# Performance work log

Measured on AMD Instinct MI355X. Metric: run time of the kernel, lower is better.

Reference implementation:

```python
import jax, jax.numpy as jnp
import numpy as np

B_, L_, H_ = 2, 2048, 2048          # batch, seq_len, hidden_size
I_, N_, NH, P_ = 4096, 128, 64, 64   # intermediate, ssm_state, num_heads, head_dim
K_, CH = 4, 256                      # conv kernel, chunk size
DT_MIN, DT_MAX = 0.0, 1e10


def setup_inputs() -> dict:
    key = jax.random.key(0)
    ks = jax.random.split(key, 8)
    conv_dim = I_ + 2 * N_
    proj_out = 2 * (I_ + N_) + NH
    return {
        "hidden_states": jax.random.normal(ks[0], (B_, L_, H_), jnp.float32),
        "W_in": jax.random.normal(ks[1], (proj_out, H_), jnp.float32) * 0.02,
        "conv_w": jax.random.normal(ks[2], (conv_dim, 1, K_), jnp.float32) * 0.2,
        "conv_b": jnp.zeros((conv_dim,), jnp.float32),
        "dt_bias": jax.random.uniform(ks[3], (NH,), jnp.float32),
        "A_log": jnp.log(jax.random.uniform(ks[4], (NH,), jnp.float32, 1.0, 16.0)),
        "D": jnp.ones((NH,), jnp.float32),
        "norm_w": jnp.ones((I_,), jnp.float32),
        "W_out": jax.random.normal(ks[5], (H_, I_), jnp.float32) * 0.02,
    }


def _segsum(x):
    # stable segment-sum: out[..., i, j] = sum_{k=j+1..i} x[..., k] for i>=j, else -inf
    T = x.shape[-1]
    xr = jnp.broadcast_to(x[..., None], x.shape + (T,))
    lower = jnp.tril(jnp.ones((T, T), bool), -1)
    s = jnp.cumsum(jnp.where(lower, xr, 0.0), axis=-2)
    return jnp.where(jnp.tril(jnp.ones((T, T), bool)), s, -jnp.inf)


def reference(hidden_states, W_in, conv_w, conv_b, dt_bias, A_log, D, norm_w, W_out):
    b, L, _ = hidden_states.shape
    proj = hidden_states @ W_in.T                       # (b, L, 2*(I+N)+H)
    z, xBC, dt = jnp.split(proj, [I_, 2 * I_ + 2 * N_], axis=-1)

    # depthwise causal conv1d + silu
    x_t = xBC.transpose(0, 2, 1)                        # (b, conv_dim, L)
    conv = jax.lax.conv_general_dilated(
        x_t, conv_w, (1,), [(K_ - 1, 0)],
        dimension_numbers=("NCH", "OIH", "NCH"), feature_group_count=I_ + 2 * N_)
    xBC = jax.nn.silu((conv + conv_b[None, :, None]).transpose(0, 2, 1))
    x, Bm, Cm = jnp.split(xBC, [I_, I_ + N_], axis=-1)  # (b,L,I) (b,L,N) (b,L,N)

    # ---- SSD naive (chunked state-space-duality scan) ----
    A = -jnp.exp(A_log.astype(jnp.float32))             # (h,)
    dt = jnp.clip(jax.nn.softplus(dt + dt_bias), DT_MIN, DT_MAX)  # (b,L,h)
    x4 = x.reshape(b, L, NH, P_)
    pad = (-L) % CH
    padf = lambda t: jnp.pad(t, [(0, 0), (0, pad)] + [(0, 0)] * (t.ndim - 2))
    D_res = D[None, None, :, None] * padf(x4)           # (b, Lp, h, p)
    xs = padf(x4 * dt[..., None])
    Ah = padf(A[None, None, :] * dt)                    # (b, Lp, h)
    Bc, Cc = padf(Bm), padf(Cm)
    c = (L + pad) // CH
    xs = xs.reshape(b, c, CH, NH, P_)                   # (b,c,l,h,p)
    Ah = Ah.reshape(b, c, CH, NH).transpose(0, 3, 1, 2) # (b,h,c,l)
    Bc = Bc.reshape(b, c, CH, N_)
    Cc = Cc.reshape(b, c, CH, N_)

    A_cs = jnp.cumsum(Ah, axis=-1)                      # (b,h,c,l)
    Lm = jnp.exp(_segsum(Ah))                           # (b,h,c,l,l)
    # intra-chunk (diagonal block) output; B/C shared across heads (n_groups=1)
    Y_diag = jnp.einsum("bcln,bcsn,bhcls,bcshp->bclhp", Cc, Bc, Lm, xs)

    decay_states = jnp.exp(A_cs[..., -1:] - A_cs)       # (b,h,c,l)
    states = jnp.einsum("bcln,bhcl,bclhp->bchpn", Bc, decay_states, xs)
    states = jnp.concatenate([jnp.zeros_like(states[:, :1]), states], axis=1)
    decay_chunk = jnp.exp(_segsum(jnp.pad(A_cs[..., -1], [(0, 0), (0, 0), (1, 0)])))
    new_states = jnp.einsum("bhzc,bchpn->bzhpn", decay_chunk, states)
    states = new_states[:, :-1]                         # (b,c,h,p,n)
    Y_off = jnp.einsum("bcln,bchpn,bhcl->bclhp", Cc, states, jnp.exp(A_cs))

    y = (Y_diag + Y_off).reshape(b, c * CH, NH, P_) + D_res
    y = y[:, :L].reshape(b, L, I_)

    # gated RMSNorm (normalize=True: multiply by silu(residual) before norm)
    yf = y.astype(jnp.float32) * jax.nn.silu(z.astype(jnp.float32))
    yf = yf * jax.lax.rsqrt(jnp.mean(yf * yf, -1, keepdims=True) + 1e-5) * norm_w
    return yf.astype(hidden_states.dtype) @ W_out.T
```

## Files before the change

kernel.cpp:

```cpp
#include <hip/hip_runtime.h>
#include <hip/hip_bf16.h>
#include <math.h>


#define B_SZ 2
#define L_SZ 2048
#define H_SZ 2048
#define I_SZ 4096
#define N_SZ 128
#define NH_SZ 64
#define P_SZ 64
#define CH_SZ 256
#define NC_SZ 8
#define PROJ_SZ 8512
#define CONV_SZ 4352
#define XOFF 4096
#define DTOFF 8448
#define BOFF 4096
#define COFF 4224

typedef __attribute__((ext_vector_type(8))) short short8_t;
typedef __attribute__((ext_vector_type(4))) float float4_t;

#define GLDS(gp, lp)                                                   \
  __builtin_amdgcn_global_load_lds(                                    \
      (const __attribute__((address_space(1))) void*)(gp),             \
      (__attribute__((address_space(3))) void*)(lp), 16, 0, 0)

__device__ __forceinline__ float bf2f(unsigned short u) {
  union { unsigned int i; float f; } v; v.i = ((unsigned int)u) << 16; return v.f;
}
__device__ __forceinline__ unsigned short f2bf(float f) {
  union { float f; unsigned int i; } v; v.f = f;
  unsigned int b = v.i + 0x7fffu + ((v.i >> 16) & 1u);
  return (unsigned short)(b >> 16);
}
__device__ __forceinline__ void unpack8(uint4 v, float* f) {
  f[0] = bf2f((unsigned short)(v.x & 0xffffu)); f[1] = bf2f((unsigned short)(v.x >> 16));
  f[2] = bf2f((unsigned short)(v.y & 0xffffu)); f[3] = bf2f((unsigned short)(v.y >> 16));
  f[4] = bf2f((unsigned short)(v.z & 0xffffu)); f[5] = bf2f((unsigned short)(v.z >> 16));
  f[6] = bf2f((unsigned short)(v.w & 0xffffu)); f[7] = bf2f((unsigned short)(v.w >> 16));
}
__device__ __forceinline__ float silu_f(float x) { return x / (1.f + expf(-x)); }

__device__ __forceinline__ float load1(const void* p, long long e, int fp32) {
  return fp32 ? ((const float*)p)[e] : bf2f(((const unsigned short*)p)[e]);
}
__device__ __forceinline__ void load4(const void* p, long long e, int fp32, float* f) {
  if (fp32) {
    float4 a = *(const float4*)((const float*)p + e);
    f[0] = a.x; f[1] = a.y; f[2] = a.z; f[3] = a.w;
  } else {
    uint2 v = *(const uint2*)((const unsigned short*)p + e);
    f[0] = bf2f((unsigned short)(v.x & 0xffffu)); f[1] = bf2f((unsigned short)(v.x >> 16));
    f[2] = bf2f((unsigned short)(v.y & 0xffffu)); f[3] = bf2f((unsigned short)(v.y >> 16));
  }
}
__device__ __forceinline__ void load8(const void* p, long long e, int fp32, float* f) {
  if (fp32) {
    float4 a = *(const float4*)((const float*)p + e);
    float4 b = *(const float4*)((const float*)p + e + 4);
    f[0] = a.x; f[1] = a.y; f[2] = a.z; f[3] = a.w;
    f[4] = b.x; f[5] = b.y; f[6] = b.z; f[7] = b.w;
  } else {
    uint4 v = *(const uint4*)((const unsigned short*)p + e);
    unpack8(v, f);
  }
}

__global__ void detect_k(const void* p0, const void* p1, const void* p2,
                         const void* p3, const void* p4, const void* p5,
                         const void* p6, const void* p7, const void* p8,
                         int n0, int n1, int n2, int n3, int n4, int n5,
                         int n6, int n7, int n8, int* flags) {
  __shared__ int pe, po;
  const void* ps[9] = {p0, p1, p2, p3, p4, p5, p6, p7, p8};
  int ns[9] = {n0, n1, n2, n3, n4, n5, n6, n7, n8};
  int t = threadIdx.x;
  for (int i = 0; i < 9; i++) {
    if (t == 0) { pe = 0; po = 0; }
    __syncthreads();
    int S = ns[i] < 256 ? ns[i] : 256;
    if (t < S) {
      unsigned short u = ((const unsigned short*)ps[i])[t];
      int ex = (u >> 7) & 0xFF;
      int plaus = ((u & 0x7FFFu) != 0) && (ex >= 0x70) && (ex <= 0x8F);
      if (plaus) { if (t & 1) atomicAdd(&po, 1); else atomicAdd(&pe, 1); }
    }
    __syncthreads();
    if (t == 0) flags[i] = (2 * pe < po) ? 1 : 0;
    __syncthreads();
  }
  if (t == 0) { flags[14] = 0; flags[15] = 0; }
}

__global__ __launch_bounds__(256)
void cvt_bf16_k(const void* __restrict__ src, unsigned short* __restrict__ dst,
                long long n8, const int* __restrict__ flags, int fi) {
  long long g = (long long)blockIdx.x * 256 + threadIdx.x;
  if (g >= n8) return;
  long long e = g * 8;
  if (flags[fi]) {
    const float* s = (const float*)src + e;
    float4 a = *(const float4*)s;
    float4 b = *(const float4*)(s + 4);
    unsigned short o[8] = {f2bf(a.x), f2bf(a.y), f2bf(a.z), f2bf(a.w),
                           f2bf(b.x), f2bf(b.y), f2bf(b.z), f2bf(b.w)};
    *(uint4*)(dst + e) = *(const uint4*)o;
  } else {
    *(uint4*)(dst + e) = *(const uint4*)((const unsigned short*)src + e);
  }
}

#define MFMA_ACC(d, a, b) \
  d = __builtin_amdgcn_mfma_f32_16x16x32_bf16(a, b, d, 0, 0, 0)
#define LDA_FR(buf, i, kk) \
  (*(const short8_t*)&As[(buf)*16384 + (wm*128 + (i)*16 + l16)*64 + \
                         (((((kk)<<2) + quad) ^ l7) << 3)])
#define LDB_FR(buf, j, kk) \
  (*(const short8_t*)&Bs[(buf)*16384 + (wn*64 + (j)*16 + l16)*64 + \
                         (((((kk)<<2) + quad) ^ l7) << 3)])
#define STAGE_A(h, tile, buf) do {                                          \
    GLDS(aSrc[h][0] + ((long long)(tile) << 6),                             \
         &As[(buf)*16384 + (h)*8192 + (wave*16)*64]);                       \
    GLDS(aSrc[h][1] + ((long long)(tile) << 6),                             \
         &As[(buf)*16384 + (h)*8192 + (wave*16 + 8)*64]);                   \
  } while (0)
#define STAGE_B(h, tile, buf) do {                                          \
    GLDS(bSrc[h][0] + ((long long)(tile) << 6),                             \
         &Bs[(buf)*16384 + (h)*8192 + (wave*16)*64]);                       \
    GLDS(bSrc[h][1] + ((long long)(tile) << 6),                             \
         &Bs[(buf)*16384 + (h)*8192 + (wave*16 + 8)*64]);                   \
  } while (0)

__global__ __launch_bounds__(512, 2)
void gemm_8ph_k(const unsigned short* __restrict__ A,
                const unsigned short* __restrict__ B,
                unsigned short* __restrict__ C,
                int N, int K, int lda, int ldb, int ldc, int gxTiles) {
  __shared__ alignas(16) unsigned short As[2 * 256 * 64];
  __shared__ alignas(16) unsigned short Bs[2 * 256 * 64];
  const int t = threadIdx.x;
  const int lane = t & 63;
  const int wave = t >> 6;
  const int quad = lane >> 4;
  const int l16 = lane & 15;
  const int l7 = lane & 7;
  const int l3 = lane >> 3;
  const int wm = wave >> 2;
  const int wn = wave & 3;

  int id = blockIdx.x;
  const int nwg = gridDim.x;
  int swz = id;
  if ((nwg & 7) == 0) swz = (id & 7) * (nwg >> 3) + (id >> 3);
  const int band = gxTiles << 2;
  const int by = (swz & 3) + ((swz / band) << 2);
  const int bx = (swz >> 2) % gxTiles;
  const int m0 = by << 8;
  const int n0 = bx << 8;
  const int NT = K >> 6;

  const int kperm = ((l7 ^ l3) << 3);
  const unsigned short* aSrc[2][2];
  const unsigned short* bSrc[2][2];
#pragma unroll
  for (int h = 0; h < 2; ++h)
#pragma unroll
    for (int c = 0; c < 2; ++c) {
      const int rloc = h * 128 + wave * 16 + c * 8 + l3;
      aSrc[h][c] = A + (long long)(m0 + rloc) * lda + kperm;
      int bn = n0 + rloc;
      if (bn > N - 1) bn = N - 1;
      bSrc[h][c] = B + (long long)bn * ldb + kperm;
    }

  float4_t acc[8][4];
#pragma unroll
  for (int i = 0; i < 8; ++i)
#pragma unroll
    for (int j = 0; j < 4; ++j) acc[i][j] = (float4_t){0.f, 0.f, 0.f, 0.f};

  STAGE_A(0, 0, 0); STAGE_A(1, 0, 0);
  STAGE_B(0, 0, 0); STAGE_B(1, 0, 0);
  STAGE_B(0, 1, 1); STAGE_B(1, 1, 1);
  asm volatile("s_waitcnt vmcnt(4)" ::: "memory");
  __builtin_amdgcn_s_barrier();

  short8_t af[4][2], bf[4][2];
  for (int tt = 0; tt < NT; ++tt) {
    const int rb = tt & 1, nb = rb ^ 1;
#pragma unroll
    for (int i = 0; i < 4; ++i) af[i][0] = LDA_FR(rb, i, 0);
#pragma unroll
    for (int j = 0; j < 4; ++j) bf[j][0] = LDB_FR(rb, j, 0);
    if (tt + 1 < NT) STAGE_A(0, tt + 1, nb);
    asm volatile("s_waitcnt lgkmcnt(4)" ::: "memory");
    __builtin_amdgcn_s_barrier();
    asm volatile("s_waitcnt lgkmcnt(0)" ::: "memory");
    __builtin_amdgcn_s_setprio(1);
#pragma unroll
    for (int i = 0; i < 4; ++i)
#pragma unroll
      for (int j = 0; j < 4; ++j) MFMA_ACC(acc[i][j], af[i][0], bf[j][0]);
    __builtin_amdgcn_s_setprio(0);
    __builtin_amdgcn_s_barrier();
#pragma unroll
    for (int i = 0; i < 4; ++i) af[i][1] = LDA_FR(rb, i, 1);
#pragma unroll
    for (int j = 0; j < 4; ++j) bf[j][1] = LDB_FR(rb, j, 1);
    if (tt + 1 < NT) STAGE_A(1, tt + 1, nb);
    asm volatile("s_waitcnt lgkmcnt(4)" ::: "memory");
    __builtin_amdgcn_s_barrier();
    asm volatile("s_waitcnt lgkmcnt(0)" ::: "memory");
    __builtin_amdgcn_s_setprio(1);
#pragma unroll
    for (int i = 0; i < 4; ++i)
#pragma unroll
      for (int j = 0; j < 4; ++j) MFMA_ACC(acc[i][j], af[i][1], bf[j][1]);
    __builtin_amdgcn_s_setprio(0);
    __builtin_amdgcn_s_barrier();
#pragma unroll
    for (int i = 0; i < 4; ++i) af[i][0] = LDA_FR(rb, 4 + i, 0);
    if (tt + 2 < NT) STAGE_B(0, tt + 2, rb);
    __builtin_amdgcn_s_barrier();
    asm volatile("s_waitcnt lgkmcnt(0)" ::: "memory");
    __builtin_amdgcn_s_setprio(1);
#pragma unroll
    for (int i = 0; i < 4; ++i)
#pragma unroll
      for (int j = 0; j < 4; ++j) MFMA_ACC(acc[4 + i][j], af[i][0], bf[j][0]);
    __builtin_amdgcn_s_setprio(0);
    __builtin_amdgcn_s_barrier();
#pragma unroll
    for (int i = 0; i < 4; ++i) af[i][1] = LDA_FR(rb, 4 + i, 1);
    if (tt + 2 < NT) STAGE_B(1, tt + 2, rb);
    __builtin_amdgcn_s_barrier();
    asm volatile("s_waitcnt lgkmcnt(0)" ::: "memory");
    __builtin_amdgcn_s_setprio(1);
#pragma unroll
    for (int i = 0; i < 4; ++i)
#pragma unroll
      for (int j = 0; j < 4; ++j) MFMA_ACC(acc[4 + i][j], af[i][1], bf[j][1]);
    __builtin_amdgcn_s_setprio(0);
    if (tt < NT - 2) asm volatile("s_waitcnt vmcnt(4)" ::: "memory");
    else             asm volatile("s_waitcnt vmcnt(0)" ::: "memory");
    __builtin_amdgcn_s_barrier();
  }

#pragma unroll
  for (int i = 0; i < 8; ++i) {
#pragma unroll
    for (int r = 0; r < 4; ++r) {
      const int m = m0 + wm * 128 + i * 16 + quad * 4 + r;
      const long long cb = (long long)m * ldc;
#pragma unroll
      for (int j = 0; j < 4; ++j) {
        const int n = n0 + wn * 64 + j * 16 + l16;
        if (n < N) C[cb + n] = f2bf(acc[i][j][r]);
      }
    }
  }
}

#define LDA2(buf, i, kk) \
  (*(const short8_t*)&As2[(buf)*8192 + (wm*64 + (i)*16 + l16)*64 + \
                          (((((kk)<<2) + quad) ^ l7) << 3)])
#define LDB2(buf, j, kk) \
  (*(const short8_t*)&Bs2[(buf)*8192 + (wn*64 + (j)*16 + l16)*64 + \
                          (((((kk)<<2) + quad) ^ l7) << 3)])

template <int OUT_MODE>
__global__ __launch_bounds__(256, 2)
void gemm_2ph_k(const unsigned short* __restrict__ A,
                const unsigned short* __restrict__ B,
                void* __restrict__ Cptr,
                int N, int K, int lda, int ldb, int ldc, int gxTiles,
                const int* __restrict__ flags, int fo) {
  __shared__ alignas(16) unsigned short As2[2 * 128 * 64];
  __shared__ alignas(16) unsigned short Bs2[2 * 128 * 64];
  const int t = threadIdx.x;
  const int lane = t & 63;
  const int wave = t >> 6;
  const int quad = lane >> 4;
  const int l16 = lane & 15;
  const int l7 = lane & 7;
  const int l3 = lane >> 3;
  const int wm = wave >> 1;
  const int wn = wave & 1;
  const int ofp = (OUT_MODE == 2) ? flags[fo] : 0;

  int id = blockIdx.x;
  const int nwg = gridDim.x;
  int swz = id;
  if ((nwg & 7) == 0) swz = (id & 7) * (nwg >> 3) + (id >> 3);
  const int band = gxTiles << 2;
  const int by = (swz & 3) + ((swz / band) << 2);
  const int bx = (swz >> 2) % gxTiles;
  const int m0 = by << 7;
  const int n0 = bx << 7;
  const int NT = K >> 6;

  const int kperm = ((l7 ^ l3) << 3);
  const unsigned short* aSrc[4];
  const unsigned short* bSrc[4];
#pragma unroll
  for (int c = 0; c < 4; ++c) {
    aSrc[c] = A + (long long)(m0 + wave * 32 + c * 8 + l3) * lda + kperm;
    int bn = n0 + wave * 32 + c * 8 + l3;
    if (bn > N - 1) bn = N - 1;
    bSrc[c] = B + (long long)bn * ldb + kperm;
  }

  float4_t acc[4][4];
#pragma unroll
  for (int i = 0; i < 4; ++i)
#pragma unroll
    for (int j = 0; j < 4; ++j) acc[i][j] = (float4_t){0.f, 0.f, 0.f, 0.f};

#pragma unroll
  for (int c = 0; c < 4; ++c) {
    GLDS(aSrc[c], &As2[(wave * 32 + c * 8) * 64]);
    GLDS(bSrc[c], &Bs2[(wave * 32 + c * 8) * 64]);
  }
  asm volatile("s_waitcnt vmcnt(0)" ::: "memory");
  __builtin_amdgcn_s_barrier();

  short8_t af[4], bfr[4];
  for (int tt = 0; tt < NT; ++tt) {
    const int rb = tt & 1, nb = rb ^ 1;
#pragma unroll
    for (int i = 0; i < 4; ++i) af[i] = LDA2(rb, i, 0);
#pragma unroll
    for (int j = 0; j < 4; ++j) bfr[j] = LDB2(rb, j, 0);
    if (tt + 1 < NT) {
      const long long ko = (long long)(tt + 1) << 6;
#pragma unroll
      for (int c = 0; c < 4; ++c) {
        GLDS(aSrc[c] + ko, &As2[nb * 8192 + (wave * 32 + c * 8) * 64]);
        GLDS(bSrc[c] + ko, &Bs2[nb * 8192 + (wave * 32 + c * 8) * 64]);
      }
    }
    __builtin_amdgcn_s_setprio(1);
#pragma unroll
    for (int i = 0; i < 4; ++i)
#pragma unroll
      for (int j = 0; j < 4; ++j) MFMA_ACC(acc[i][j], af[i], bfr[j]);
    __builtin_amdgcn_s_setprio(0);
#pragma unroll
    for (int i = 0; i < 4; ++i) af[i] = LDA2(rb, i, 1);
#pragma unroll
    for (int j = 0; j < 4; ++j) bfr[j] = LDB2(rb, j, 1);
    __builtin_amdgcn_s_setprio(1);
#pragma unroll
    for (int i = 0; i < 4; ++i)
#pragma unroll
      for (int j = 0; j < 4; ++j) MFMA_ACC(acc[i][j], af[i], bfr[j]);
    __builtin_amdgcn_s_setprio(0);
    asm volatile("s_waitcnt vmcnt(0)" ::: "memory");
    __builtin_amdgcn_s_barrier();
  }

#pragma unroll
  for (int i = 0; i < 4; ++i) {
#pragma unroll
    for (int r = 0; r < 4; ++r) {
      const int m = m0 + wm * 64 + i * 16 + quad * 4 + r;
      const long long cb = (long long)m * ldc;
#pragma unroll
      for (int j = 0; j < 4; ++j) {
        const int n = n0 + wn * 64 + j * 16 + l16;
        if (n < N) {
          float v = acc[i][j][r];
          if (ofp) ((float*)Cptr)[cb + n] = v;
          else     ((unsigned short*)Cptr)[cb + n] = f2bf(v);
        }
      }
    }
  }
}

template <int OUT_MODE>
__global__ __launch_bounds__(256)
void gemm_bt_k(const void* __restrict__ A, const void* __restrict__ B,
               void* __restrict__ Cptr, int M, int N, int K,
               int lda, int ldb, int ldc,
               long long sA, long long sB, long long sC,
               const int* __restrict__ flags, int fa, int fb, int fo) {
  __shared__ float As[128][20];
  __shared__ float Bs[128][20];
  const int t = threadIdx.x;
  const int tx = t & 15, ty = t >> 4;
  const int m0 = blockIdx.y * 128, n0 = blockIdx.x * 128;
  const int afp = flags[fa], bfp = flags[fb];
  const int ofp = (OUT_MODE == 2) ? flags[fo] : (OUT_MODE == 1);
  const long long zoff = (long long)blockIdx.z;
  float* Cf = (float*)Cptr + zoff * sC;
  unsigned short* Cb = (unsigned short*)Cptr + zoff * sC;

  float acc[8][8];
#pragma unroll
  for (int i = 0; i < 8; i++)
#pragma unroll
    for (int j = 0; j < 8; j++) acc[i][j] = 0.f;

  const int rowS = t >> 1;
  const int kof  = (t & 1) * 8;
  const long long aRow = zoff * sA + (long long)(m0 + rowS) * lda + kof;
  const long long bRow = zoff * sB + (long long)(n0 + rowS) * ldb + kof;
  const bool bOK = (n0 + rowS) < N;

  for (int k0 = 0; k0 < K; k0 += 16) {
    float af[8], bf[8];
    load8(A, aRow + k0, afp, af);
    if (bOK) load8(B, bRow + k0, bfp, bf);
    else { bf[0]=bf[1]=bf[2]=bf[3]=bf[4]=bf[5]=bf[6]=bf[7]=0.f; }
    __syncthreads();
    *(float4*)&As[rowS][kof]     = make_float4(af[0], af[1], af[2], af[3]);
    *(float4*)&As[rowS][kof + 4] = make_float4(af[4], af[5], af[6], af[7]);
    *(float4*)&Bs[rowS][kof]     = make_float4(bf[0], bf[1], bf[2], bf[3]);
    *(float4*)&Bs[rowS][kof + 4] = make_float4(bf[4], bf[5], bf[6], bf[7]);
    __syncthreads();
#pragma unroll
    for (int kk = 0; kk < 16; kk += 2) {
      float2 a2[8], b2[8];
#pragma unroll
      for (int i = 0; i < 8; i++) a2[i] = *(const float2*)&As[ty + 16 * i][kk];
#pragma unroll
      for (int j = 0; j < 8; j++) b2[j] = *(const float2*)&Bs[tx + 16 * j][kk];
#pragma unroll
      for (int i = 0; i < 8; i++)
#pragma unroll
        for (int j = 0; j < 8; j++) {
          acc[i][j] = fmaf(a2[i].x, b2[j].x, acc[i][j]);
          acc[i][j] = fmaf(a2[i].y, b2[j].y, acc[i][j]);
        }
    }
  }
#pragma unroll
  for (int i = 0; i < 8; i++) {
    const int m = m0 + ty + 16 * i;
    const long long base = (long long)m * ldc;
#pragma unroll
    for (int j = 0; j < 8; j++) {
      const int n = n0 + tx + 16 * j;
      if (n < N) {
        if (ofp) Cf[base + n] = acc[i][j];
        else     Cb[base + n] = f2bf(acc[i][j]);
      }
    }
  }
}

__global__ __launch_bounds__(256)
void conv_silu_k(const unsigned short* __restrict__ proj,
                 const void* __restrict__ cw,
                 const void* __restrict__ cb,
                 unsigned short* __restrict__ convx,
                 const int* __restrict__ flags) {
  const int total = B_SZ * L_SZ * (CONV_SZ / 4);
  int g = blockIdx.x * 256 + threadIdx.x;
  if (g >= total) return;
  const int fw = flags[2], fb = flags[3];
  int c4 = g % (CONV_SZ / 4);
  int bl = g / (CONV_SZ / 4);
  int l = bl & (L_SZ - 1);
  int ch = c4 * 4;
  float w0[8], w1[8];
  load8(cw, (long long)ch * 4, fw, w0);
  load8(cw, (long long)ch * 4 + 8, fw, w1);
  float accv[4];
  load4(cb, ch, fb, accv);
  float acc0 = accv[0], acc1 = accv[1], acc2 = accv[2], acc3 = accv[3];
  const long long rb = (long long)(bl - l);
#pragma unroll
  for (int k = 0; k < 4; k++) {
    int ls = l - 3 + k;
    if (ls < 0) continue;
    uint2 xv = *(const uint2*)(proj + (rb + ls) * PROJ_SZ + XOFF + ch);
    float x0 = bf2f((unsigned short)(xv.x & 0xffffu));
    float x1 = bf2f((unsigned short)(xv.x >> 16));
    float x2 = bf2f((unsigned short)(xv.y & 0xffffu));
    float x3 = bf2f((unsigned short)(xv.y >> 16));
    acc0 = fmaf(x0, w0[k], acc0);
    acc1 = fmaf(x1, w0[4 + k], acc1);
    acc2 = fmaf(x2, w1[k], acc2);
    acc3 = fmaf(x3, w1[4 + k], acc3);
  }
  unsigned short o0 = f2bf(silu_f(acc0));
  unsigned short o1 = f2bf(silu_f(acc1));
  unsigned short o2 = f2bf(silu_f(acc2));
  unsigned short o3 = f2bf(silu_f(acc3));
  *(uint2*)(convx + (long long)bl * CONV_SZ + ch) =
      make_uint2((unsigned int)o0 | ((unsigned int)o1 << 16),
                 (unsigned int)o2 | ((unsigned int)o3 << 16));
}

__global__ __launch_bounds__(256)
void dt_prep_k(const unsigned short* __restrict__ proj,
               const void* __restrict__ dt_bias,
               float* __restrict__ dtv, const int* __restrict__ flags) {
  int g = blockIdx.x * 256 + threadIdx.x;
  int h = g & 63;
  long long bl = g >> 6;
  float v = bf2f(proj[bl * PROJ_SZ + DTOFF + h]) + load1(dt_bias, h, flags[4]);
  float sp = (v > 20.f) ? v : log1pf(expf(v));
  dtv[g] = sp;
}

__global__ __launch_bounds__(256)
void acs_scan_k(const float* __restrict__ dtv,
                const void* __restrict__ A_log,
                float* __restrict__ acs, const int* __restrict__ flags) {
  __shared__ float sd[256];
  int blk = blockIdx.x;
  int h = blk & 63;
  int bc = blk >> 6;
  int l = threadIdx.x;
  float Ah = -expf(load1(A_log, h, flags[5]));
  long long row = (long long)bc * CH_SZ + l;
  sd[l] = Ah * dtv[row * NH_SZ + h];
  for (int off = 1; off < 256; off <<= 1) {
    __syncthreads();
    float tv = (l >= off) ? sd[l - off] : 0.f;
    __syncthreads();
    sd[l] += tv;
  }
  acs[(long long)blk * CH_SZ + l] = sd[l];
}

__global__ __launch_bounds__(256)
void chunk_states_k(const unsigned short* __restrict__ convx,
                    const float* __restrict__ dtv,
                    const float* __restrict__ acs,
                    float* __restrict__ stc) {
  __shared__ float Bw[32][128];
  __shared__ float xw[32][64];
  int blk = blockIdx.x;
  int h = blk & 63;
  int bc = blk >> 6;
  int t = threadIdx.x;
  const int p0 = (t & 15) * 4, n0 = (t >> 4) * 8;
  const float* acsb = acs + (long long)blk * 256;
  const float alast = acsb[255];
  float acc[4][8];
#pragma unroll
  for (int i = 0; i < 4; i++)
#pragma unroll
    for (int j = 0; j < 8; j++) acc[i][j] = 0.f;
  const long long row0 = (long long)bc * 256;

  for (int lt0 = 0; lt0 < 256; lt0 += 32) {
    __syncthreads();
#pragma unroll
    for (int q = 0; q < 4; q++) {
      int idx4 = (t + 256 * q) * 4;
      int r = idx4 >> 7, n = idx4 & 127;
      uint2 v = *(const uint2*)(convx + (row0 + lt0 + r) * CONV_SZ + BOFF + n);
      Bw[r][n]     = bf2f((unsigned short)(v.x & 0xffffu));
      Bw[r][n + 1] = bf2f((unsigned short)(v.x >> 16));
      Bw[r][n + 2] = bf2f((unsigned short)(v.y & 0xffffu));
      Bw[r][n + 3] = bf2f((unsigned short)(v.y >> 16));
    }
#pragma unroll
    for (int q = 0; q < 2; q++) {
      int idx4 = (t + 256 * q) * 4;
      int r = idx4 >> 6, p = idx4 & 63;
      long long lg = row0 + lt0 + r;
      float sc = dtv[lg * NH_SZ + h] * expf(alast - acsb[lt0 + r]);
      uint2 v = *(const uint2*)(convx + lg * CONV_SZ + h * 64 + p);
      xw[r][p]     = bf2f((unsigned short)(v.x & 0xffffu)) * sc;
      xw[r][p + 1] = bf2f((unsigned short)(v.x >> 16)) * sc;
      xw[r][p + 2] = bf2f((unsigned short)(v.y & 0xffffu)) * sc;
      xw[r][p + 3] = bf2f((unsigned short)(v.y >> 16)) * sc;
    }
    __syncthreads();
#pragma unroll 4
    for (int lt = 0; lt < 32; lt++) {
      float4 xv = *(const float4*)&xw[lt][p0];
      float4 b0 = *(const float4*)&Bw[lt][n0];
      float4 b1 = *(const float4*)&Bw[lt][n0 + 4];
      float xa[4] = {xv.x, xv.y, xv.z, xv.w};
      float ba[8] = {b0.x, b0.y, b0.z, b0.w, b1.x, b1.y, b1.z, b1.w};
#pragma unroll
      for (int i = 0; i < 4; i++)
#pragma unroll
        for (int j = 0; j < 8; j++) acc[i][j] = fmaf(xa[i], ba[j], acc[i][j]);
    }
  }
  float* outb = stc + (long long)blk * 8192;
#pragma unroll
  for (int i = 0; i < 4; i++) {
    *(float4*)&outb[(p0 + i) * 128 + n0] =
        make_float4(acc[i][0], acc[i][1], acc[i][2], acc[i][3]);
    *(float4*)&outb[(p0 + i) * 128 + n0 + 4] =
        make_float4(acc[i][4], acc[i][5], acc[i][6], acc[i][7]);
  }
}

__global__ __launch_bounds__(256)
void recur_k(float* __restrict__ stc, const float* __restrict__ acs) {
  int blk = blockIdx.x;
  int b = blk >> 6, h = blk & 63;
  int t = threadIdx.x;
  float S[32];
#pragma unroll
  for (int j = 0; j < 32; j++) S[j] = 0.f;
  for (int z = 0; z < 8; z++) {
    long long bz = ((long long)b * 8 + z) * 64 + h;
    long long base = bz * 8192;
    float e = expf(acs[bz * 256 + 255]);
#pragma unroll
    for (int j = 0; j < 32; j++) {
      int idx = j * 256 + t;
      float cs = stc[base + idx];
      stc[base + idx] = S[j];
      S[j] = fmaf(e, S[j], cs);
    }
  }
}

__global__ __launch_bounds__(256)
void yoff_k(const unsigned short* __restrict__ convx,
            const float* __restrict__ sti,
            const float* __restrict__ acs,
            const void* __restrict__ Dw,
            float* __restrict__ y, const int* __restrict__ flags) {
  __shared__ float SIt[128][68];
  __shared__ unsigned short Ct[64][128];
  int blk = blockIdx.x;
  int h = blk & 63;
  int bc = blk >> 6;
  int t = threadIdx.x;
  const int txp = t & 15, lq = t >> 4;
  const float Dh = load1(Dw, h, flags[6]);
  const float* sib = sti + (long long)blk * 8192;
#pragma unroll 4
  for (int q = 0; q < 32; q++) {
    int idx = t + 256 * q;
    SIt[idx & 127][idx >> 7] = sib[idx];
  }
  const float* acsb = acs + (long long)blk * 256;
  const long long row0 = (long long)bc * 256;
  for (int ltile = 0; ltile < 4; ltile++) {
    __syncthreads();
#pragma unroll 4
    for (int q = 0; q < 32; q++) {
      int idx = t + 256 * q;
      int lr = idx >> 7, n = idx & 127;
      Ct[lr][n] = convx[(row0 + ltile * 64 + lr) * CONV_SZ + COFF + n];
    }
    __syncthreads();
    float acc[4][4] = {};
#pragma unroll 4
    for (int n = 0; n < 128; n++) {
      float4 sv = *(const float4*)&SIt[n][txp * 4];
      float c0 = bf2f(Ct[lq * 4 + 0][n]);
      float c1 = bf2f(Ct[lq * 4 + 1][n]);
      float c2 = bf2f(Ct[lq * 4 + 2][n]);
      float c3 = bf2f(Ct[lq * 4 + 3][n]);
      acc[0][0] = fmaf(c0, sv.x, acc[0][0]); acc[0][1] = fmaf(c0, sv.y, acc[0][1]);
      acc[0][2] = fmaf(c0, sv.z, acc[0][2]); acc[0][3] = fmaf(c0, sv.w, acc[0][3]);
      acc[1][0] = fmaf(c1, sv.x, acc[1][0]); acc[1][1] = fmaf(c1, sv.y, acc[1][1]);
      acc[1][2] = fmaf(c1, sv.z, acc[1][2]); acc[1][3] = fmaf(c1, sv.w, acc[1][3]);
      acc[2][0] = fmaf(c2, sv.x, acc[2][0]); acc[2][1] = fmaf(c2, sv.y, acc[2][1]);
      acc[2][2] = fmaf(c2, sv.z, acc[2][2]); acc[2][3] = fmaf(c2, sv.w, acc[2][3]);
      acc[3][0] = fmaf(c3, sv.x, acc[3][0]); acc[3][1] = fmaf(c3, sv.y, acc[3][1]);
      acc[3][2] = fmaf(c3, sv.z, acc[3][2]); acc[3][3] = fmaf(c3, sv.w, acc[3][3]);
    }
#pragma unroll
    for (int i = 0; i < 4; i++) {
      int lloc = ltile * 64 + lq * 4 + i;
      long long row = row0 + lloc;
      float ex = expf(acsb[lloc]);
      uint2 xv = *(const uint2*)(convx + row * CONV_SZ + h * 64 + txp * 4);
      float4 o;
      o.x = fmaf(ex, acc[i][0], Dh * bf2f((unsigned short)(xv.x & 0xffffu)));
      o.y = fmaf(ex, acc[i][1], Dh * bf2f((unsigned short)(xv.x >> 16)));
      o.z = fmaf(ex, acc[i][2], Dh * bf2f((unsigned short)(xv.y & 0xffffu)));
      o.w = fmaf(ex, acc[i][3], Dh * bf2f((unsigned short)(xv.y >> 16)));
      *(float4*)&y[row * I_SZ + h * 64 + txp * 4] = o;
    }
  }
}

__global__ __launch_bounds__(256)
void ydiag_k(const unsigned short* __restrict__ convx,
             const float* __restrict__ dtv,
             const float* __restrict__ acs,
             const float* __restrict__ Gmat,
             float* __restrict__ y) {
  __shared__ float acs_s[256];
  __shared__ float xsT[64][68];
  __shared__ float Mt[64][66];
  int blk = blockIdx.x;
  int h = blk & 63;
  int bc = blk >> 6;
  int t = threadIdx.x;
  const int txp = t & 15, lq = t >> 4;
  acs_s[t] = acs[(long long)blk * 256 + t];
  const long long row0 = (long long)bc * 256;
  const float* Gb = Gmat + (long long)bc * 65536;
  for (int ltile = 0; ltile < 4; ltile++) {
    float acc[4][4] = {};
    for (int stile = 0; stile <= ltile; stile++) {
      __syncthreads();
#pragma unroll 4
      for (int q = 0; q < 16; q++) {
        int idx = t + 256 * q;
        int ss = idx >> 6, p = idx & 63;
        long long row = row0 + stile * 64 + ss;
        xsT[ss][p] = bf2f(convx[row * CONV_SZ + h * 64 + p]) * dtv[row * NH_SZ + h];
      }
#pragma unroll 4
      for (int q = 0; q < 16; q++) {
        int idx = t + 256 * q;
        int lr = idx >> 6, ss = idx & 63;
        int lg = ltile * 64 + lr, sg = stile * 64 + ss;
        float m = 0.f;
        if (sg <= lg) m = Gb[(long long)lg * 256 + sg] * expf(acs_s[lg] - acs_s[sg]);
        Mt[lr][ss] = m;
      }
      __syncthreads();
#pragma unroll 4
      for (int ss = 0; ss < 64; ss++) {
        float4 xv = *(const float4*)&xsT[ss][txp * 4];
        float m0 = Mt[lq * 4 + 0][ss];
        float m1 = Mt[lq * 4 + 1][ss];
        float m2 = Mt[lq * 4 + 2][ss];
        float m3 = Mt[lq * 4 + 3][ss];
        acc[0][0] = fmaf(m0, xv.x, acc[0][0]); acc[0][1] = fmaf(m0, xv.y, acc[0][1]);
        acc[0][2] = fmaf(m0, xv.z, acc[0][2]); acc[0][3] = fmaf(m0, xv.w, acc[0][3]);
        acc[1][0] = fmaf(m1, xv.x, acc[1][0]); acc[1][1] = fmaf(m1, xv.y, acc[1][1]);
        acc[1][2] = fmaf(m1, xv.z, acc[1][2]); acc[1][3] = fmaf(m1, xv.w, acc[1][3]);
        acc[2][0] = fmaf(m2, xv.x, acc[2][0]); acc[2][1] = fmaf(m2, xv.y, acc[2][1]);
        acc[2][2] = fmaf(m2, xv.z, acc[2][2]); acc[2][3] = fmaf(m2, xv.w, acc[2][3]);
        acc[3][0] = fmaf(m3, xv.x, acc[3][0]); acc[3][1] = fmaf(m3, xv.y, acc[3][1]);
        acc[3][2] = fmaf(m3, xv.z, acc[3][2]); acc[3][3] = fmaf(m3, xv.w, acc[3][3]);
      }
    }
#pragma unroll
    for (int i = 0; i < 4; i++) {
      long long row = row0 + ltile * 64 + lq * 4 + i;
      float* yp = &y[row * I_SZ + h * 64 + txp * 4];
      float4 cur = *(float4*)yp;
      cur.x += acc[i][0]; cur.y += acc[i][1]; cur.z += acc[i][2]; cur.w += acc[i][3];
      *(float4*)yp = cur;
    }
  }
}

__global__ __launch_bounds__(256)
void norm_k(const float* __restrict__ y,
            const unsigned short* __restrict__ proj,
            const void* __restrict__ nw,
            unsigned short* __restrict__ yfb, const int* __restrict__ flags) {
  __shared__ float red[4];
  __shared__ float sc_s;
  int row = blockIdx.x;
  int t = threadIdx.x;
  const int fn = flags[7];
  const float* yr = y + (long long)row * I_SZ;
  const unsigned short* zr = proj + (long long)row * PROJ_SZ;
  float g[16];
  float ss = 0.f;
#pragma unroll
  for (int q = 0; q < 4; q++) {
    int i0 = q * 1024 + t * 4;
    float4 yv = *(const float4*)&yr[i0];
    uint2 zv = *(const uint2*)&zr[i0];
    float z0 = bf2f((unsigned short)(zv.x & 0xffffu));
    float z1 = bf2f((unsigned short)(zv.x >> 16));
    float z2 = bf2f((unsigned short)(zv.y & 0xffffu));
    float z3 = bf2f((unsigned short)(zv.y >> 16));
    float g0 = yv.x * silu_f(z0), g1 = yv.y * silu_f(z1);
    float g2 = yv.z * silu_f(z2), g3 = yv.w * silu_f(z3);
    g[q * 4 + 0] = g0; g[q * 4 + 1] = g1; g[q * 4 + 2] = g2; g[q * 4 + 3] = g3;
    ss += g0 * g0 + g1 * g1 + g2 * g2 + g3 * g3;
  }
#pragma unroll
  for (int off = 32; off > 0; off >>= 1) ss += __shfl_down(ss, off, 64);
  if ((t & 63) == 0) red[t >> 6] = ss;
  __syncthreads();
  if (t == 0) sc_s = rsqrtf((red[0] + red[1] + red[2] + red[3]) * (1.f / 4096.f) + 1e-5f);
  __syncthreads();
  float sc = sc_s;
#pragma unroll
  for (int q = 0; q < 4; q++) {
    int i0 = q * 1024 + t * 4;
    float nv[4];
    load4(nw, i0, fn, nv);
    unsigned short o0 = f2bf(g[q * 4 + 0] * sc * nv[0]);
    unsigned short o1 = f2bf(g[q * 4 + 1] * sc * nv[1]);
    unsigned short o2 = f2bf(g[q * 4 + 2] * sc * nv[2]);
    unsigned short o3 = f2bf(g[q * 4 + 3] * sc * nv[3]);
    *(uint2*)&yfb[(long long)row * I_SZ + i0] =
        make_uint2((unsigned int)o0 | ((unsigned int)o1 << 16),
                   (unsigned int)o2 | ((unsigned int)o3 << 16));
  }
}

extern "C" void kernel_launch(void* const* d_in, const int* in_sizes, int n_in,
                              void* d_out, int out_size, void* d_ws, size_t ws_size,
                              hipStream_t stream) {
  const void* hs     = d_in[0];
  const void* W_in   = d_in[1];
  const void* conv_w = d_in[2];
  const void* conv_b = d_in[3];
  const void* dt_b   = d_in[4];
  const void* A_log  = d_in[5];
  const void* Dw     = d_in[6];
  const void* nw     = d_in[7];
  const void* W_out  = d_in[8];

  char* ws = (char*)d_ws;
  size_t off = 0;
  auto alloc = [&](size_t bytes) -> void* {
    void* p = ws + off;
    off += (bytes + 255) & ~(size_t)255;
    return p;
  };
  const long long ML = (long long)B_SZ * L_SZ;
  int* flags = (int*)alloc(64);
  unsigned short* proj  = (unsigned short*)alloc(ML * PROJ_SZ * 2);
  unsigned short* convx = (unsigned short*)alloc(ML * CONV_SZ * 2);
  float* dtv  = (float*)alloc(ML * NH_SZ * 4);
  float* acsb = (float*)alloc((long long)B_SZ * NC_SZ * NH_SZ * CH_SZ * 4);
  float* Gm   = (float*)alloc((long long)B_SZ * NC_SZ * CH_SZ * CH_SZ * 4);
  float* stc  = (float*)alloc((long long)B_SZ * NC_SZ * NH_SZ * P_SZ * N_SZ * 4);
  float* yb   = (float*)alloc(ML * I_SZ * 4);
  unsigned short* yfb = (unsigned short*)stc;
  unsigned short* hs_bf   = (unsigned short*)yb;
  unsigned short* Win_bf  = (unsigned short*)yb + 8388608;
  unsigned short* Wout_bf = (unsigned short*)yb;
  (void)n_in; (void)out_size;
  if (off > ws_size) return;

  dim3 blk(256);
  detect_k<<<1, blk, 0, stream>>>(hs, W_in, conv_w, conv_b, dt_b, A_log, Dw, nw, W_out,
                                  in_sizes[0], in_sizes[1], in_sizes[2], in_sizes[3],
                                  in_sizes[4], in_sizes[5], in_sizes[6], in_sizes[7],
                                  in_sizes[8], flags);
  cvt_bf16_k<<<dim3(4096), blk, 0, stream>>>(hs, hs_bf, 1048576LL, flags, 0);
  cvt_bf16_k<<<dim3(8512), blk, 0, stream>>>(W_in, Win_bf, 2179072LL, flags, 1);
  gemm_8ph_k<<<dim3(512), dim3(512), 0, stream>>>(
      hs_bf, Win_bf, proj, PROJ_SZ, H_SZ, H_SZ, H_SZ, PROJ_SZ, 32);
  gemm_2ph_k<0><<<dim3(96), blk, 0, stream>>>(
      hs_bf, Win_bf + 8192LL * 2048, proj + 8192, 320, H_SZ,
      H_SZ, H_SZ, PROJ_SZ, 3, flags, 15);
  conv_silu_k<<<dim3((B_SZ * L_SZ * (CONV_SZ / 4) + 255) / 256), blk, 0, stream>>>(
      proj, conv_w, conv_b, convx, flags);
  dt_prep_k<<<dim3((unsigned)(ML * NH_SZ / 256)), blk, 0, stream>>>(proj, dt_b, dtv, flags);
  acs_scan_k<<<dim3(B_SZ * NC_SZ * NH_SZ), blk, 0, stream>>>(dtv, A_log, acsb, flags);
  gemm_bt_k<1><<<dim3(2, 2, 16), blk, 0, stream>>>(
      (const unsigned short*)convx + COFF, (const unsigned short*)convx + BOFF,
      Gm, 256, 256, 128, CONV_SZ, CONV_SZ, 256,
      (long long)256 * CONV_SZ, (long long)256 * CONV_SZ, 65536,
      flags, 15, 15, 15);
  chunk_states_k<<<dim3(1024), blk, 0, stream>>>(convx, dtv, acsb, stc);
  recur_k<<<dim3(B_SZ * NH_SZ), blk, 0, stream>>>(stc, acsb);
  yoff_k<<<dim3(1024), blk, 0, stream>>>(convx, stc, acsb, Dw, yb, flags);
  ydiag_k<<<dim3(1024), blk, 0, stream>>>(convx, dtv, acsb, Gm, yb);
  norm_k<<<dim3((unsigned)ML), blk, 0, stream>>>(yb, proj, nw, yfb, flags);
  cvt_bf16_k<<<dim3(4096), blk, 0, stream>>>(W_out, Wout_bf, 1048576LL, flags, 8);
  gemm_2ph_k<2><<<dim3(512), blk, 0, stream>>>(
      yfb, Wout_bf, d_out, H_SZ, I_SZ, I_SZ, I_SZ, H_SZ, 16,
      flags, 0);
}
```

Before: 726.9 us.

## Use MFMA for C·B Gram matrix and off-diagonal state output kernels

Replaces the FP32 SIMT tiled GEMM that computes the per-chunk C·Bᵀ Gram matrix with an MFMA kernel that loads bf16 fragments straight from global memory. The Y_off kernel is likewise rewritten to use MFMA, converting the fp32 inter-chunk states to bf16 on the fly instead of staging them transposed in shared memory. This is meant to cut FMA-bound time in two medium-sized GEMMs. In exchange it drops shared-memory reuse, uses less coalesced scalar stores, and rounds the states to bf16, which costs some accuracy.

```diff
diff --git a/kernel.cpp b/kernel.cpp
--- a/kernel.cpp
+++ b/kernel.cpp
@@ -66,6 +66,16 @@
     uint4 v = *(const uint4*)((const unsigned short*)p + e);
     unpack8(v, f);
   }
+}
+__device__ __forceinline__ short8_t pack_bf8(const float* p) {
+  float4 a = *(const float4*)p;
+  float4 b = *(const float4*)(p + 4);
+  short8_t r;
+  r[0] = (short)f2bf(a.x); r[1] = (short)f2bf(a.y);
+  r[2] = (short)f2bf(a.z); r[3] = (short)f2bf(a.w);
+  r[4] = (short)f2bf(b.x); r[5] = (short)f2bf(b.y);
+  r[6] = (short)f2bf(b.z); r[7] = (short)f2bf(b.w);
+  return r;
 }
 
 __global__ void detect_k(const void* p0, const void* p1, const void* p2,
@@ -380,76 +390,50 @@
   }
 }
 
-template <int OUT_MODE>
-__global__ __launch_bounds__(256)
-void gemm_bt_k(const void* __restrict__ A, const void* __restrict__ B,
-               void* __restrict__ Cptr, int M, int N, int K,
-               int lda, int ldb, int ldc,
-               long long sA, long long sB, long long sC,
-               const int* __restrict__ flags, int fa, int fb, int fo) {
-  __shared__ float As[128][20];
-  __shared__ float Bs[128][20];
+__global__ __launch_bounds__(256)
+void gemm_g_k(const unsigned short* __restrict__ convx,
+              float* __restrict__ Gm) {
   const int t = threadIdx.x;
-  const int tx = t & 15, ty = t >> 4;
-  const int m0 = blockIdx.y * 128, n0 = blockIdx.x * 128;
-  const int afp = flags[fa], bfp = flags[fb];
-  const int ofp = (OUT_MODE == 2) ? flags[fo] : (OUT_MODE == 1);
-  const long long zoff = (long long)blockIdx.z;
-  float* Cf = (float*)Cptr + zoff * sC;
-  unsigned short* Cb = (unsigned short*)Cptr + zoff * sC;
-
-  float acc[8][8];
-#pragma unroll
-  for (int i = 0; i < 8; i++)
-#pragma unroll
-    for (int j = 0; j < 8; j++) acc[i][j] = 0.f;
-
-  const int rowS = t >> 1;
-  const int kof  = (t & 1) * 8;
-  const long long aRow = zoff * sA + (long long)(m0 + rowS) * lda + kof;
-  const long long bRow = zoff * sB + (long long)(n0 + rowS) * ldb + kof;
-  const bool bOK = (n0 + rowS) < N;
-
-  for (int k0 = 0; k0 < K; k0 += 16) {
-    float af[8], bf[8];
-    load8(A, aRow + k0, afp, af);
-    if (bOK) load8(B, bRow + k0, bfp, bf);
-    else { bf[0]=bf[1]=bf[2]=bf[3]=bf[4]=bf[5]=bf[6]=bf[7]=0.f; }
-    __syncthreads();
-    *(float4*)&As[rowS][kof]     = make_float4(af[0], af[1], af[2], af[3]);
-    *(float4*)&As[rowS][kof + 4] = make_float4(af[4], af[5], af[6], af[7]);
-    *(float4*)&Bs[rowS][kof]     = make_float4(bf[0], bf[1], bf[2], bf[3]);
-    *(float4*)&Bs[rowS][kof + 4] = make_float4(bf[4], bf[5], bf[6], bf[7]);
-    __syncthreads();
-#pragma unroll
-    for (int kk = 0; kk < 16; kk += 2) {
-      float2 a2[8], b2[8];
-#pragma unroll
-      for (int i = 0; i < 8; i++) a2[i] = *(const float2*)&As[ty + 16 * i][kk];
-#pragma unroll
-      for (int j = 0; j < 8; j++) b2[j] = *(const float2*)&Bs[tx + 16 * j][kk];
-#pragma unroll
-      for (int i = 0; i < 8; i++)
-#pragma unroll
-        for (int j = 0; j < 8; j++) {
-          acc[i][j] = fmaf(a2[i].x, b2[j].x, acc[i][j]);
-          acc[i][j] = fmaf(a2[i].y, b2[j].y, acc[i][j]);
-        }
-    }
-  }
-#pragma unroll
-  for (int i = 0; i < 8; i++) {
-    const int m = m0 + ty + 16 * i;
-    const long long base = (long long)m * ldc;
-#pragma unroll
-    for (int j = 0; j < 8; j++) {
-      const int n = n0 + tx + 16 * j;
-      if (n < N) {
-        if (ofp) Cf[base + n] = acc[i][j];
-        else     Cb[base + n] = f2bf(acc[i][j]);
-      }
-    }
-  }
+  const int lane = t & 63;
+  const int wave = t >> 6;
+  const int quad = lane >> 4;
+  const int l16 = lane & 15;
+  const int wm = wave >> 1, wn = wave & 1;
+  const int m0 = blockIdx.y * 128 + wm * 64;
+  const int n0 = blockIdx.x * 128 + wn * 64;
+  const long long row0 = (long long)blockIdx.z * 256;
+
+  float4_t acc[4][4];
+#pragma unroll
+  for (int i = 0; i < 4; ++i)
+#pragma unroll
+    for (int j = 0; j < 4; ++j) acc[i][j] = (float4_t){0.f, 0.f, 0.f, 0.f};
+
+#pragma unroll
+  for (int kt = 0; kt < 4; ++kt) {
+    const int ko = kt * 32 + quad * 8;
+    short8_t a[4], b[4];
+#pragma unroll
+    for (int i = 0; i < 4; ++i)
+      a[i] = *(const short8_t*)&convx[(row0 + m0 + i * 16 + l16) * CONV_SZ + COFF + ko];
+#pragma unroll
+    for (int j = 0; j < 4; ++j)
+      b[j] = *(const short8_t*)&convx[(row0 + n0 + j * 16 + l16) * CONV_SZ + BOFF + ko];
+#pragma unroll
+    for (int i = 0; i < 4; ++i)
+#pragma unroll
+      for (int j = 0; j < 4; ++j) MFMA_ACC(acc[i][j], a[i], b[j]);
+  }
+  float* Gb = Gm + (long long)blockIdx.z * 65536;
+#pragma unroll
+  for (int i = 0; i < 4; ++i)
+#pragma unroll
+    for (int r = 0; r < 4; ++r) {
+      const int m = m0 + i * 16 + quad * 4 + r;
+#pragma unroll
+      for (int j = 0; j < 4; ++j)
+        Gb[(long long)m * 256 + n0 + j * 16 + l16] = acc[i][j][r];
+    }
 }
 
 __global__ __launch_bounds__(256)
@@ -621,65 +605,61 @@
 }
 
 __global__ __launch_bounds__(256)
-void yoff_k(const unsigned short* __restrict__ convx,
-            const float* __restrict__ sti,
-            const float* __restrict__ acs,
-            const void* __restrict__ Dw,
-            float* __restrict__ y, const int* __restrict__ flags) {
-  __shared__ float SIt[128][68];
-  __shared__ unsigned short Ct[64][128];
-  int blk = blockIdx.x;
-  int h = blk & 63;
-  int bc = blk >> 6;
-  int t = threadIdx.x;
-  const int txp = t & 15, lq = t >> 4;
+void yoff_mfma_k(const unsigned short* __restrict__ convx,
+                 const float* __restrict__ sti,
+                 const float* __restrict__ acs,
+                 const void* __restrict__ Dw,
+                 float* __restrict__ y, const int* __restrict__ flags) {
+  const int blk = blockIdx.x;
+  const int h = blk & 63;
+  const int bc = blk >> 6;
+  const int t = threadIdx.x;
+  const int lane = t & 63;
+  const int wave = t >> 6;
+  const int quad = lane >> 4;
+  const int l16 = lane & 15;
+  const int l0 = wave * 64;
+  const long long row0 = (long long)bc * 256;
+  const float* sib = sti + (long long)blk * 8192;
+  const float* acsb = acs + (long long)blk * 256;
   const float Dh = load1(Dw, h, flags[6]);
-  const float* sib = sti + (long long)blk * 8192;
-#pragma unroll 4
-  for (int q = 0; q < 32; q++) {
-    int idx = t + 256 * q;
-    SIt[idx & 127][idx >> 7] = sib[idx];
-  }
-  const float* acsb = acs + (long long)blk * 256;
-  const long long row0 = (long long)bc * 256;
-  for (int ltile = 0; ltile < 4; ltile++) {
-    __syncthreads();
-#pragma unroll 4
-    for (int q = 0; q < 32; q++) {
-      int idx = t + 256 * q;
-      int lr = idx >> 7, n = idx & 127;
-      Ct[lr][n] = convx[(row0 + ltile * 64 + lr) * CONV_SZ + COFF + n];
-    }
-    __syncthreads();
-    float acc[4][4] = {};
-#pragma unroll 4
-    for (int n = 0; n < 128; n++) {
-      float4 sv = *(const float4*)&SIt[n][txp * 4];
-      float c0 = bf2f(Ct[lq * 4 + 0][n]);
-      float c1 = bf2f(Ct[lq * 4 + 1][n]);
-      float c2 = bf2f(Ct[lq * 4 + 2][n]);
-      float c3 = bf2f(Ct[lq * 4 + 3][n]);
-      acc[0][0] = fmaf(c0, sv.x, acc[0][0]); acc[0][1] = fmaf(c0, sv.y, acc[0][1]);
-      acc[0][2] = fmaf(c0, sv.z, acc[0][2]); acc[0][3] = fmaf(c0, sv.w, acc[0][3]);
-      acc[1][0] = fmaf(c1, sv.x, acc[1][0]); acc[1][1] = fmaf(c1, sv.y, acc[1][1]);
-      acc[1][2] = fmaf(c1, sv.z, acc[1][2]); acc[1][3] = fmaf(c1, sv.w, acc[1][3]);
-      acc[2][0] = fmaf(c2, sv.x, acc[2][0]); acc[2][1] = fmaf(c2, sv.y, acc[2][1]);
-      acc[2][2] = fmaf(c2, sv.z, acc[2][2]); acc[2][3] = fmaf(c2, sv.w, acc[2][3]);
-      acc[3][0] = fmaf(c3, sv.x, acc[3][0]); acc[3][1] = fmaf(c3, sv.y, acc[3][1]);
-      acc[3][2] = fmaf(c3, sv.z, acc[3][2]); acc[3][3] = fmaf(c3, sv.w, acc[3][3]);
-    }
-#pragma unroll
-    for (int i = 0; i < 4; i++) {
-      int lloc = ltile * 64 + lq * 4 + i;
-      long long row = row0 + lloc;
-      float ex = expf(acsb[lloc]);
-      uint2 xv = *(const uint2*)(convx + row * CONV_SZ + h * 64 + txp * 4);
-      float4 o;
-      o.x = fmaf(ex, acc[i][0], Dh * bf2f((unsigned short)(xv.x & 0xffffu)));
-      o.y = fmaf(ex, acc[i][1], Dh * bf2f((unsigned short)(xv.x >> 16)));
-      o.z = fmaf(ex, acc[i][2], Dh * bf2f((unsigned short)(xv.y & 0xffffu)));
-      o.w = fmaf(ex, acc[i][3], Dh * bf2f((unsigned short)(xv.y >> 16)));
-      *(float4*)&y[row * I_SZ + h * 64 + txp * 4] = o;
+
+  float4_t acc[4][4];
+#pragma unroll
+  for (int i = 0; i < 4; ++i)
+#pragma unroll
+    for (int j = 0; j < 4; ++j) acc[i][j] = (float4_t){0.f, 0.f, 0.f, 0.f};
+
+#pragma unroll
+  for (int kt = 0; kt < 4; ++kt) {
+    const int ko = kt * 32 + quad * 8;
+    short8_t a[4], b[4];
+#pragma unroll
+    for (int i = 0; i < 4; ++i)
+      a[i] = *(const short8_t*)&convx[(row0 + l0 + i * 16 + l16) * CONV_SZ + COFF + ko];
+#pragma unroll
+    for (int j = 0; j < 4; ++j)
+      b[j] = pack_bf8(sib + (j * 16 + l16) * 128 + ko);
+#pragma unroll
+    for (int i = 0; i < 4; ++i)
+#pragma unroll
+      for (int j = 0; j < 4; ++j) MFMA_ACC(acc[i][j], a[i], b[j]);
+  }
+
+#pragma unroll
+  for (int i = 0; i < 4; ++i) {
+#pragma unroll
+    for (int r = 0; r < 4; ++r) {
+      const int m = l0 + i * 16 + quad * 4 + r;
+      const long long row = row0 + m;
+      const float ex = expf(acsb[m]);
+      const unsigned short* xr = convx + row * CONV_SZ + h * 64;
+      float* yr = y + row * I_SZ + h * 64;
+#pragma unroll
+      for (int j = 0; j < 4; ++j) {
+        const int p = j * 16 + l16;
+        yr[p] = fmaf(ex, acc[i][j][r], Dh * bf2f(xr[p]));
+      }
     }
   }
 }
@@ -852,14 +832,10 @@
       proj, conv_w, conv_b, convx, flags);
   dt_prep_k<<<dim3((unsigned)(ML * NH_SZ / 256)), blk, 0, stream>>>(proj, dt_b, dtv, flags);
   acs_scan_k<<<dim3(B_SZ * NC_SZ * NH_SZ), blk, 0, stream>>>(dtv, A_log, acsb, flags);
-  gemm_bt_k<1><<<dim3(2, 2, 16), blk, 0, stream>>>(
-      (const unsigned short*)convx + COFF, (const unsigned short*)convx + BOFF,
-      Gm, 256, 256, 128, CONV_SZ, CONV_SZ, 256,
-      (long long)256 * CONV_SZ, (long long)256 * CONV_SZ, 65536,
-      flags, 15, 15, 15);
+  gemm_g_k<<<dim3(2, 2, 16), blk, 0, stream>>>(convx, Gm);
   chunk_states_k<<<dim3(1024), blk, 0, stream>>>(convx, dtv, acsb, stc);
   recur_k<<<dim3(B_SZ * NH_SZ), blk, 0, stream>>>(stc, acsb);
-  yoff_k<<<dim3(1024), blk, 0, stream>>>(convx, stc, acsb, Dw, yb, flags);
+  yoff_mfma_k<<<dim3(1024), blk, 0, stream>>>(convx, stc, acsb, Dw, yb, flags);
   ydiag_k<<<dim3(1024), blk, 0, stream>>>(convx, dtv, acsb, Gm, yb);
   norm_k<<<dim3((unsigned)ML), blk, 0, stream>>>(yb, proj, nw, yfb, flags);
   cvt_bf16_k<<<dim3(4096), blk, 0, stream>>>(W_out, Wout_bf, 1048576LL, flags, 8);
```

Measured after the change: 677.8 us. 1.07x faster.
